# Performance work log

Measured on AMD Instinct MI355X. Metric: run time of the kernel, lower is better.

The kernel has to match this reference:

```python
import jax, jax.numpy as jnp
import numpy as np

N, D, E = 100000, 128, 1600000
BN_EPS = 1e-5

def setup_inputs() -> dict:
    key = jax.random.key(0)
    k1, k2, k3 = jax.random.split(key, 3)
    src_embeddings = jax.random.normal(k1, (N, D), dtype=jnp.float32)
    dst_embeddings = jax.random.normal(k2, (N, D), dtype=jnp.float32)
    graph = jax.random.randint(k3, (2, E), 0, N, dtype=jnp.int64)
    bn_weight = jnp.ones((1,), dtype=jnp.float32)
    bn_bias = jnp.zeros((1,), dtype=jnp.float32)
    return {
        "src_embeddings": src_embeddings,
        "dst_embeddings": dst_embeddings,
        "graph": graph,
        "bn_weight": bn_weight,
        "bn_bias": bn_bias,
    }

def reference(src_embeddings, dst_embeddings, graph, bn_weight, bn_bias):
    # gather endpoint embeddings by edge indices: [E, D]
    src = src_embeddings[graph[0]]
    dst = dst_embeddings[graph[1]]
    # squared distance per edge, clamped as in torch .clamp(min=1e-12)
    d2 = jnp.clip(jnp.sum((src - dst) ** 2, axis=-1), 1e-12, None)  # [E]
    likelihood = -jnp.log(d2)
    # BatchNorm1d(1) in training mode: batch mean, biased variance, eps=1e-5
    mu = jnp.mean(likelihood)
    var = jnp.mean((likelihood - mu) ** 2)
    edge_weights_logits = bn_weight[0] * (likelihood - mu) * jax.lax.rsqrt(var + BN_EPS) + bn_bias[0]
    # weighting_function = torch.sigmoid
    edge_weights = jax.nn.sigmoid(edge_weights_logits)
    # normalize=True: divide by mean
    edge_weights = edge_weights / jnp.mean(edge_weights)
    edge_weights = edge_weights[:, None]  # [E, 1]
    return graph, edge_weights, edge_weights_logits
```

## Files before the change

kernel.cpp:

```cpp
#include <hip/hip_runtime.h>
#include <math.h>

#define EMB_D 128
#define BN_EPS 1e-5f
#define GATHER_BLOCKS 2048
#define OVF_CAP 8192

typedef float v2f __attribute__((ext_vector_type(2)));

#if defined(__has_builtin)
#if __has_builtin(__builtin_amdgcn_cvt_pk_f32_fp8) && __has_builtin(__builtin_amdgcn_cvt_pk_fp8_f32)
#define FP8_HW 1
#endif
#endif

__device__ __forceinline__ unsigned int sw_f32_to_fp8(float x) {
    unsigned int u = __float_as_uint(x);
    unsigned int s = u >> 31;
    int e = (int)((u >> 23) & 0xff) - 127;
    unsigned int m = u & 0x7fffff;
    m += 0x7FFFF + ((m >> 20) & 1);
    if (m >> 23) { m = 0; e += 1; }
    int e8 = e + 7;
    if (e8 <= 0) return s << 7;
    if (e8 >= 15) return (s << 7) | 0x7E;
    return (s << 7) | ((unsigned)e8 << 3) | (m >> 20);
}

__device__ __forceinline__ float sw_fp8_to_f32(unsigned int v) {
    unsigned int s = (v >> 7) & 1, e = (v >> 3) & 15, m = v & 7;
    if (e == 0) return 0.0f;
    unsigned int bits = (s << 31) | ((e - 7 + 127) << 23) | (m << 20);
    return __uint_as_float(bits);
}

__device__ __forceinline__ unsigned int pack4_fp8(float4 v) {
#ifdef FP8_HW
    unsigned int o = 0;
    o = (unsigned int)__builtin_amdgcn_cvt_pk_fp8_f32(v.x, v.y, (int)o, false);
    o = (unsigned int)__builtin_amdgcn_cvt_pk_fp8_f32(v.z, v.w, (int)o, true);
    return o;
#else
    return sw_f32_to_fp8(v.x) | (sw_f32_to_fp8(v.y) << 8) |
           (sw_f32_to_fp8(v.z) << 16) | (sw_f32_to_fp8(v.w) << 24);
#endif
}

__device__ __forceinline__ float fp8x4_d2(unsigned int ua, unsigned int ub) {
#ifdef FP8_HW
    v2f a0 = __builtin_amdgcn_cvt_pk_f32_fp8((int)ua, false);
    v2f a1 = __builtin_amdgcn_cvt_pk_f32_fp8((int)ua, true);
    v2f b0 = __builtin_amdgcn_cvt_pk_f32_fp8((int)ub, false);
    v2f b1 = __builtin_amdgcn_cvt_pk_f32_fp8((int)ub, true);
    float dx = a0.x - b0.x, dy = a0.y - b0.y;
    float dz = a1.x - b1.x, dw = a1.y - b1.y;
#else
    float dx = sw_fp8_to_f32(ua & 0xff)         - sw_fp8_to_f32(ub & 0xff);
    float dy = sw_fp8_to_f32((ua >> 8) & 0xff)  - sw_fp8_to_f32((ub >> 8) & 0xff);
    float dz = sw_fp8_to_f32((ua >> 16) & 0xff) - sw_fp8_to_f32((ub >> 16) & 0xff);
    float dw = sw_fp8_to_f32(ua >> 24)          - sw_fp8_to_f32(ub >> 24);
#endif
    return fmaf(dx, dx, fmaf(dy, dy, fmaf(dz, dz, dw * dw)));
}

__device__ __forceinline__ float chunk_d2(uint4 a, uint4 b) {
    return fp8x4_d2(a.x, b.x) + fp8x4_d2(a.y, b.y)
         + fp8x4_d2(a.z, b.z) + fp8x4_d2(a.w, b.w);
}

__device__ __forceinline__ float edge_L(const unsigned char* src8,
                                        const unsigned char* dst8,
                                        int s, int d, int sub) {
    const uint4* sa = (const uint4*)(src8 + (long long)s * 128) + sub * 4;
    const uint4* sb = (const uint4*)(dst8 + (long long)d * 128) + sub * 4;
    const uint4 a0 = sa[0], a1 = sa[1], a2 = sa[2], a3 = sa[3];
    const uint4 b0 = sb[0], b1 = sb[1], b2 = sb[2], b3 = sb[3];
    float p = chunk_d2(a0, b0) + chunk_d2(a1, b1)
            + chunk_d2(a2, b2) + chunk_d2(a3, b3);
    p += __shfl_xor(p, 1, 64);
    return -logf(fmaxf(p, 1e-12f));
}

__device__ __forceinline__ unsigned int flat_to_rec(unsigned int f,
                                                    const unsigned int (&pre)[9],
                                                    unsigned int cap) {
    unsigned int j = 0, pj = 0;
    #pragma unroll
    for (int k = 1; k < 8; ++k) {
        const bool ge = (f >= pre[k]);
        j  = ge ? (unsigned int)k : j;
        pj = ge ? pre[k] : pj;
    }
    return j * cap + (f - pj);
}

__global__ void prep_bin_kernel(const float* __restrict__ src,
                                const float* __restrict__ dst,
                                unsigned int* __restrict__ src8,
                                unsigned int* __restrict__ dst8,
                                long long nElem,
                                const int* __restrict__ g,
                                long long E,
                                float* __restrict__ out_graph,
                                unsigned long long* __restrict__ rec,
                                unsigned int* __restrict__ cursors,
                                unsigned int cap,
                                float inv_slice)
{
    {
        const long long nthreads = (long long)gridDim.x * blockDim.x;
        const long long tid0 = (long long)blockIdx.x * blockDim.x + threadIdx.x;
        const long long nvec = nElem / 4;
        for (long long i = tid0; i < nvec; i += nthreads)
            src8[i] = pack4_fp8(((const float4*)src)[i]);
        for (long long i = tid0; i < nvec; i += nthreads)
            dst8[i] = pack4_fp8(((const float4*)dst)[i]);
    }

    __shared__ unsigned int hist[64];
    __shared__ unsigned int curs[64];

    const long long chunkSz = (long long)blockDim.x * 8;
    const long long nchunks = (E + chunkSz - 1) / chunkSz;

    for (long long c = blockIdx.x; c < nchunks; c += gridDim.x) {
        const long long base = c * chunkSz;
        if (threadIdx.x < 64) hist[threadIdx.x] = 0;
        __syncthreads();

        int bb[8];
        unsigned long long pk[8];
        #pragma unroll
        for (int k = 0; k < 8; ++k) {
            const long long e = base + (long long)k * blockDim.x + threadIdx.x;
            bb[k] = -1;
            if (e < E) {
                const unsigned int s = (unsigned int)g[e];
                const unsigned int d = (unsigned int)g[E + e];
                out_graph[e]     = (float)s;
                out_graph[E + e] = (float)d;
                int bs = (int)((float)s * inv_slice); bs = bs > 7 ? 7 : bs;
                int bd = (int)((float)d * inv_slice); bd = bd > 7 ? 7 : bd;
                bb[k] = bs * 8 + bd;
                pk[k] = (unsigned long long)s | ((unsigned long long)d << 20)
                      | ((unsigned long long)e << 40);
                atomicAdd(&hist[bb[k]], 1u);
            }
        }
        __syncthreads();
        if (threadIdx.x < 64 && hist[threadIdx.x] > 0)
            curs[threadIdx.x] = atomicAdd(&cursors[threadIdx.x], hist[threadIdx.x]);
        __syncthreads();

        #pragma unroll
        for (int k = 0; k < 8; ++k) {
            if (bb[k] >= 0) {
                unsigned int off = atomicAdd(&curs[bb[k]], 1u);
                if (off < cap) {
                    rec[(unsigned int)bb[k] * cap + off] = pk[k];
                } else {
                    unsigned int oo = atomicAdd(&cursors[64], 1u);
                    if (oo < OVF_CAP) rec[64u * cap + oo] = pk[k];
                }
            }
        }
        __syncthreads();
    }
}

__global__ void edge_l_binned2_kernel(const unsigned char* __restrict__ src8,
                                      const unsigned char* __restrict__ dst8,
                                      const unsigned long long* __restrict__ rec,
                                      const unsigned int* __restrict__ cursors,
                                      unsigned int cap,
                                      float* __restrict__ l_out,
                                      double* __restrict__ acc)
{
    const int tid = threadIdx.x;
    const int sub = tid & 7;
    const int grp = tid >> 3;
    const int xcd = blockIdx.x & 7;
    const unsigned int local = blockIdx.x >> 3;
    const unsigned int nloc  = gridDim.x >> 3;

    unsigned int pre[9];
    pre[0] = 0;
    #pragma unroll
    for (int j = 0; j < 8; ++j) {
        unsigned int c = cursors[xcd * 8 + j];
        if (c > cap) c = cap;
        pre[j + 1] = pre[j] + c;
    }
    const unsigned int M = pre[8];
    const unsigned long long recBase = (unsigned long long)(xcd * 8) * cap;

    double sumL = 0.0, sumL2 = 0.0;

    const unsigned int perBlock = 64;
    const unsigned int stride = nloc * perBlock;

    for (unsigned int f0 = local * perBlock; f0 < M; f0 += stride) {
        const unsigned int f1 = f0 + (unsigned int)grp;
        const unsigned int f2 = f1 + 32u;
        const bool ok1 = f1 < M;
        const bool ok2 = f2 < M;

        unsigned long long v1 = 0ull, v2 = 0ull;
        if (ok1) v1 = rec[recBase + flat_to_rec(f1, pre, cap)];
        if (ok2) v2 = rec[recBase + flat_to_rec(f2, pre, cap)];

        const int s1 = (int)(v1 & 0xFFFFFu);
        const int d1 = (int)((v1 >> 20) & 0xFFFFFu);
        const int s2 = (int)(v2 & 0xFFFFFu);
        const int d2i = (int)((v2 >> 20) & 0xFFFFFu);

        const uint4 A1 = ((const uint4*)(src8 + (long long)s1 * 128))[sub];
        const uint4 B1 = ((const uint4*)(dst8 + (long long)d1 * 128))[sub];
        const uint4 A2 = ((const uint4*)(src8 + (long long)s2 * 128))[sub];
        const uint4 B2 = ((const uint4*)(dst8 + (long long)d2i * 128))[sub];

        float p1 = chunk_d2(A1, B1);
        float p2 = chunk_d2(A2, B2);

        p1 += __shfl_xor(p1, 1, 64);
        p1 += __shfl_xor(p1, 2, 64);
        p1 += __shfl_xor(p1, 4, 64);
        p2 += __shfl_xor(p2, 1, 64);
        p2 += __shfl_xor(p2, 2, 64);
        p2 += __shfl_xor(p2, 4, 64);

        if (sub == 0) {
            if (ok1) {
                const float L = -logf(fmaxf(p1, 1e-12f));
                __builtin_nontemporal_store(L, &l_out[(long long)(v1 >> 40)]);
                sumL  += (double)L;
                sumL2 += (double)L * (double)L;
            }
            if (ok2) {
                const float L = -logf(fmaxf(p2, 1e-12f));
                __builtin_nontemporal_store(L, &l_out[(long long)(v2 >> 40)]);
                sumL  += (double)L;
                sumL2 += (double)L * (double)L;
            }
        }
    }

    {
        unsigned int ovfN = cursors[64];
        if (ovfN > OVF_CAP) ovfN = OVF_CAP;
        const unsigned long long obase = 64ull * cap;
        const unsigned int gstride = gridDim.x * 32u;
        for (unsigned int f = blockIdx.x * 32u + (unsigned int)grp;
             f < ovfN; f += gstride) {
            const unsigned long long v = rec[obase + f];
            const int s = (int)(v & 0xFFFFFu);
            const int d = (int)((v >> 20) & 0xFFFFFu);
            const uint4 A = ((const uint4*)(src8 + (long long)s * 128))[sub];
            const uint4 B = ((const uint4*)(dst8 + (long long)d * 128))[sub];
            float p = chunk_d2(A, B);
            p += __shfl_xor(p, 1, 64);
            p += __shfl_xor(p, 2, 64);
            p += __shfl_xor(p, 4, 64);
            if (sub == 0) {
                const float L = -logf(fmaxf(p, 1e-12f));
                __builtin_nontemporal_store(L, &l_out[(long long)(v >> 40)]);
                sumL  += (double)L;
                sumL2 += (double)L * (double)L;
            }
        }
    }

    __shared__ double sA[256];
    __shared__ double sB[256];
    sA[tid] = sumL;
    sB[tid] = sumL2;
    __syncthreads();
    for (int ofs = 128; ofs >= 1; ofs >>= 1) {
        if (tid < ofs) {
            sA[tid] += sA[tid + ofs];
            sB[tid] += sB[tid + ofs];
        }
        __syncthreads();
    }
    if (tid == 0) {
        atomicAdd(&acc[0], sA[0]);
        atomicAdd(&acc[1], sB[0]);
    }
}

__global__ void prep_tables_kernel(const float* __restrict__ src,
                                   const float* __restrict__ dst,
                                   unsigned int* __restrict__ src8,
                                   unsigned int* __restrict__ dst8,
                                   long long nElem)
{
    const long long nthreads = (long long)gridDim.x * blockDim.x;
    const long long tid0 = (long long)blockIdx.x * blockDim.x + threadIdx.x;
    const long long nvec = nElem / 4;
    for (long long i = tid0; i < nvec; i += nthreads)
        src8[i] = pack4_fp8(((const float4*)src)[i]);
    for (long long i = tid0; i < nvec; i += nthreads)
        dst8[i] = pack4_fp8(((const float4*)dst)[i]);
}

__global__ void edge_l_fp8_kernel(const unsigned char* __restrict__ src8,
                                  const unsigned char* __restrict__ dst8,
                                  const int* __restrict__ g,
                                  long long E,
                                  float*  __restrict__ l_out,
                                  double* __restrict__ acc)
{
    const int sub = threadIdx.x & 1;
    const int eg  = threadIdx.x >> 1;
    const long long stride = (long long)gridDim.x * 128;

    double sumL = 0.0, sumL2 = 0.0;

    long long e = (long long)blockIdx.x * 128 + eg;
    int s = 0, d = 0;
    if (e < E) { s = g[e]; d = g[E + e]; }

    while (e < E) {
        const long long en = e + stride;
        int sn = 0, dn = 0;
        if (en < E) { sn = g[en]; dn = g[E + en]; }
        const float L = edge_L(src8, dst8, s, d, sub);
        if (sub == 0) {
            l_out[e] = L;
            sumL  += (double)L;
            sumL2 += (double)L * (double)L;
        }
        e = en; s = sn; d = dn;
    }

    __shared__ double sA[256];
    __shared__ double sB[256];
    sA[threadIdx.x] = sumL;
    sB[threadIdx.x] = sumL2;
    __syncthreads();
    for (int ofs = 128; ofs >= 1; ofs >>= 1) {
        if ((int)threadIdx.x < ofs) {
            sA[threadIdx.x] += sA[threadIdx.x + ofs];
            sB[threadIdx.x] += sB[threadIdx.x + ofs];
        }
        __syncthreads();
    }
    if (threadIdx.x == 0) {
        atomicAdd(&acc[0], sA[0]);
        atomicAdd(&acc[1], sB[0]);
    }
}

__global__ void edge_l_kernel(const float* __restrict__ src,
                              const float* __restrict__ dst,
                              const int*   __restrict__ g,
                              long long E,
                              float*  __restrict__ l_out,
                              double* __restrict__ acc)
{
    const int sub  = threadIdx.x & 7;
    const int egrp = threadIdx.x >> 3;
    const long long stride = (long long)gridDim.x * 32;

    double sumL = 0.0, sumL2 = 0.0;

    long long e = (long long)blockIdx.x * 32 + egrp;
    int s = 0, d = 0;
    if (e < E) { s = g[e]; d = g[E + e]; }

    while (e < E) {
        const long long en = e + stride;
        int sn = 0, dn = 0;
        if (en < E) { sn = g[en]; dn = g[E + en]; }

        const float4* sa = (const float4*)(src + (long long)s * EMB_D);
        const float4* sb = (const float4*)(dst + (long long)d * EMB_D);
        const float4 a0 = sa[sub];      const float4 b0 = sb[sub];
        const float4 a1 = sa[sub + 8];  const float4 b1 = sb[sub + 8];
        const float4 a2 = sa[sub + 16]; const float4 b2 = sb[sub + 16];
        const float4 a3 = sa[sub + 24]; const float4 b3 = sb[sub + 24];

        float dx, dy, dz, dw, p = 0.f;
        dx = a0.x-b0.x; dy = a0.y-b0.y; dz = a0.z-b0.z; dw = a0.w-b0.w;
        p += fmaf(dx,dx,fmaf(dy,dy,fmaf(dz,dz,dw*dw)));
        dx = a1.x-b1.x; dy = a1.y-b1.y; dz = a1.z-b1.z; dw = a1.w-b1.w;
        p += fmaf(dx,dx,fmaf(dy,dy,fmaf(dz,dz,dw*dw)));
        dx = a2.x-b2.x; dy = a2.y-b2.y; dz = a2.z-b2.z; dw = a2.w-b2.w;
        p += fmaf(dx,dx,fmaf(dy,dy,fmaf(dz,dz,dw*dw)));
        dx = a3.x-b3.x; dy = a3.y-b3.y; dz = a3.z-b3.z; dw = a3.w-b3.w;
        p += fmaf(dx,dx,fmaf(dy,dy,fmaf(dz,dz,dw*dw)));

        p += __shfl_xor(p, 1, 64);
        p += __shfl_xor(p, 2, 64);
        p += __shfl_xor(p, 4, 64);

        if (sub == 0) {
            const float L = -logf(fmaxf(p, 1e-12f));
            l_out[e] = L;
            sumL  += (double)L;
            sumL2 += (double)L * (double)L;
        }
        e = en; s = sn; d = dn;
    }

    __shared__ double sA[256];
    __shared__ double sB[256];
    sA[threadIdx.x] = sumL;
    sB[threadIdx.x] = sumL2;
    __syncthreads();
    for (int ofs = 128; ofs >= 1; ofs >>= 1) {
        if ((int)threadIdx.x < ofs) {
            sA[threadIdx.x] += sA[threadIdx.x + ofs];
            sB[threadIdx.x] += sB[threadIdx.x + ofs];
        }
        __syncthreads();
    }
    if (threadIdx.x == 0) {
        atomicAdd(&acc[0], sA[0]);
        atomicAdd(&acc[1], sB[0]);
    }
}

__global__ void bn_sig_kernel(float* __restrict__ logits,
                              float* __restrict__ ew,
                              const double* __restrict__ acc,
                              double* __restrict__ sig_acc,
                              const float* __restrict__ bn_w,
                              const float* __restrict__ bn_b,
                              long long E)
{
    const long long nthreads = (long long)gridDim.x * blockDim.x;
    const long long tid0 = (long long)blockIdx.x * blockDim.x + threadIdx.x;

    __shared__ float s_mu, s_inv, s_w, s_b;
    if (threadIdx.x == 0) {
        const double mu  = acc[0] / (double)E;
        const double var = acc[1] / (double)E - mu * mu;
        s_mu  = (float)mu;
        s_inv = (float)(1.0 / sqrt(var + (double)BN_EPS));
        s_w   = bn_w[0];
        s_b   = bn_b[0];
    }
    __syncthreads();
    const float mu = s_mu, inv = s_inv, w = s_w, b = s_b;

    double sig = 0.0;
    const long long nvec = E / 4;
    for (long long i = tid0; i < nvec; i += nthreads) {
        float4 L = ((const float4*)logits)[i];
        float4 z;
        z.x = w * (L.x - mu) * inv + b;
        z.y = w * (L.y - mu) * inv + b;
        z.z = w * (L.z - mu) * inv + b;
        z.w = w * (L.w - mu) * inv + b;
        ((float4*)logits)[i] = z;
        float4 sg;
        sg.x = 1.0f / (1.0f + expf(-z.x));
        sg.y = 1.0f / (1.0f + expf(-z.y));
        sg.z = 1.0f / (1.0f + expf(-z.z));
        sg.w = 1.0f / (1.0f + expf(-z.w));
        ((float4*)ew)[i] = sg;
        sig += (double)(sg.x + sg.y) + (double)(sg.z + sg.w);
    }
    for (long long i = nvec * 4 + tid0; i < E; i += nthreads) {
        const float L = logits[i];
        const float z = w * (L - mu) * inv + b;
        logits[i] = z;
        const float sg = 1.0f / (1.0f + expf(-z));
        ew[i] = sg;
        sig += (double)sg;
    }

    __shared__ double sS[256];
    sS[threadIdx.x] = sig;
    __syncthreads();
    for (int ofs = 128; ofs >= 1; ofs >>= 1) {
        if ((int)threadIdx.x < ofs)
            sS[threadIdx.x] += sS[threadIdx.x + ofs];
        __syncthreads();
    }
    if (threadIdx.x == 0)
        atomicAdd(sig_acc, sS[0]);
}

__global__ void norm_kernel(float* __restrict__ ew,
                            const double* __restrict__ sig_acc,
                            const int* __restrict__ g,
                            float* __restrict__ out_graph,
                            int do_graph,
                            long long E)
{
    const long long nthreads = (long long)gridDim.x * blockDim.x;
    const long long tid0 = (long long)blockIdx.x * blockDim.x + threadIdx.x;
    const float scale = (float)((double)E / sig_acc[0]);

    const long long nvec = E / 4;
    for (long long i = tid0; i < nvec; i += nthreads) {
        float4 v = ((const float4*)ew)[i];
        v.x *= scale; v.y *= scale; v.z *= scale; v.w *= scale;
        ((float4*)ew)[i] = v;
    }
    for (long long i = nvec * 4 + tid0; i < E; i += nthreads)
        ew[i] *= scale;

    if (do_graph) {
        const long long gvec = (2 * E) / 4;
        for (long long i = tid0; i < gvec; i += nthreads) {
            const int4 v = ((const int4*)g)[i];
            float4 f;
            f.x = (float)v.x; f.y = (float)v.y; f.z = (float)v.z; f.w = (float)v.w;
            ((float4*)out_graph)[i] = f;
        }
        for (long long i = gvec * 4 + tid0; i < 2 * E; i += nthreads)
            out_graph[i] = (float)g[i];
    }
}

extern "C" void kernel_launch(void* const* d_in, const int* in_sizes, int n_in,
                              void* d_out, int out_size, void* d_ws, size_t ws_size,
                              hipStream_t stream) {
    const float* src  = (const float*)d_in[0];
    const float* dst  = (const float*)d_in[1];
    const int*   g    = (const int*)d_in[2];
    const float* bn_w = (const float*)d_in[3];
    const float* bn_b = (const float*)d_in[4];

    const long long N = (long long)in_sizes[0] / EMB_D;
    const long long E = (long long)in_sizes[2] / 2;

    float* out        = (float*)d_out;
    float* out_graph  = out;
    float* out_ew     = out + 2 * E;
    float* out_logits = out + 3 * E;

    double*       acc     = (double*)d_ws;
    unsigned int* cursors = (unsigned int*)((char*)d_ws + 64);
    unsigned char* src8   = (unsigned char*)d_ws + 512;
    unsigned char* dst8   = src8 + (size_t)N * EMB_D;
    unsigned long long* rec = (unsigned long long*)(dst8 + (size_t)N * EMB_D);

    const unsigned int cap = (unsigned int)(E / 64 + 2048);
    const size_t need_full = 512 + (size_t)N * EMB_D * 2
                           + ((size_t)64 * cap + OVF_CAP) * 8;
    const size_t need_fp8  = 512 + (size_t)N * EMB_D * 2;

    const int slice_sz = (int)((N + 7) / 8);
    const float inv_slice = 1.0f / (float)slice_sz;

    hipMemsetAsync(d_ws, 0, 512, stream);

    if (ws_size >= need_full && N < (1 << 20) && E < (1LL << 24)) {
        prep_bin_kernel<<<4096, 256, 0, stream>>>(src, dst,
                                                  (unsigned int*)src8,
                                                  (unsigned int*)dst8,
                                                  N * EMB_D, g, E, out_graph,
                                                  rec, cursors, cap, inv_slice);
        edge_l_binned2_kernel<<<GATHER_BLOCKS, 256, 0, stream>>>(
            src8, dst8, rec, cursors, cap, out_logits, acc);
        bn_sig_kernel<<<1024, 256, 0, stream>>>(out_logits, out_ew, acc, &acc[2],
                                                bn_w, bn_b, E);
        norm_kernel<<<1024, 256, 0, stream>>>(out_ew, &acc[2], g, out_graph, 0, E);
    } else if (ws_size >= need_fp8) {
        prep_tables_kernel<<<4096, 256, 0, stream>>>(src, dst,
                                                     (unsigned int*)src8,
                                                     (unsigned int*)dst8,
                                                     N * EMB_D);
        edge_l_fp8_kernel<<<4096, 256, 0, stream>>>(src8, dst8, g, E,
                                                    out_logits, acc);
        bn_sig_kernel<<<1024, 256, 0, stream>>>(out_logits, out_ew, acc, &acc[2],
                                                bn_w, bn_b, E);
        norm_kernel<<<1024, 256, 0, stream>>>(out_ew, &acc[2], g, out_graph, 1, E);
    } else {
        edge_l_kernel<<<4096, 256, 0, stream>>>(src, dst, g, E, out_logits, acc);
        bn_sig_kernel<<<1024, 256, 0, stream>>>(out_logits, out_ew, acc, &acc[2],
                                                bn_w, bn_b, E);
        norm_kernel<<<1024, 256, 0, stream>>>(out_ew, &acc[2], g, out_graph, 1, E);
    }
}
```

Baseline: 262.6 us.

## Unroll binned gather to four edges, recompute sigmoid in normalize pass

The binned gather kernel now processes four edges per 8-lane group per iteration instead of two, with twice the grid size, so more independent gathers are in flight. The BN/sigmoid kernel no longer writes sigmoid values and only accumulates their sum. The normalize kernel then recomputes the sigmoid from the logits and writes scaled weights with nontemporal stores. Graph output writes in the binning kernel also become nontemporal. This trades one extra exp per element for one fewer E-sized write and read pass, at the cost of more register pressure in the gather kernel.

```diff
diff --git a/kernel.cpp b/kernel.cpp
--- a/kernel.cpp
+++ b/kernel.cpp
@@ -3,10 +3,11 @@
 
 #define EMB_D 128
 #define BN_EPS 1e-5f
-#define GATHER_BLOCKS 2048
+#define GATHER_BLOCKS 4096
 #define OVF_CAP 8192
 
 typedef float v2f __attribute__((ext_vector_type(2)));
+typedef float v4f __attribute__((ext_vector_type(4)));
 
 #if defined(__has_builtin)
 #if __has_builtin(__builtin_amdgcn_cvt_pk_f32_fp8) && __has_builtin(__builtin_amdgcn_cvt_pk_fp8_f32)
@@ -137,8 +138,8 @@
             if (e < E) {
                 const unsigned int s = (unsigned int)g[e];
                 const unsigned int d = (unsigned int)g[E + e];
-                out_graph[e]     = (float)s;
-                out_graph[E + e] = (float)d;
+                __builtin_nontemporal_store((float)s, &out_graph[e]);
+                __builtin_nontemporal_store((float)d, &out_graph[E + e]);
                 int bs = (int)((float)s * inv_slice); bs = bs > 7 ? 7 : bs;
                 int bd = (int)((float)d * inv_slice); bd = bd > 7 ? 7 : bd;
                 bb[k] = bs * 8 + bd;
@@ -168,7 +169,7 @@
     }
 }
 
-__global__ void edge_l_binned2_kernel(const unsigned char* __restrict__ src8,
+__global__ void edge_l_binned3_kernel(const unsigned char* __restrict__ src8,
                                       const unsigned char* __restrict__ dst8,
                                       const unsigned long long* __restrict__ rec,
                                       const unsigned int* __restrict__ cursors,
@@ -196,51 +197,51 @@
 
     double sumL = 0.0, sumL2 = 0.0;
 
-    const unsigned int perBlock = 64;
+    const unsigned int perBlock = 128;
     const unsigned int stride = nloc * perBlock;
 
     for (unsigned int f0 = local * perBlock; f0 < M; f0 += stride) {
-        const unsigned int f1 = f0 + (unsigned int)grp;
-        const unsigned int f2 = f1 + 32u;
-        const bool ok1 = f1 < M;
-        const bool ok2 = f2 < M;
-
-        unsigned long long v1 = 0ull, v2 = 0ull;
-        if (ok1) v1 = rec[recBase + flat_to_rec(f1, pre, cap)];
-        if (ok2) v2 = rec[recBase + flat_to_rec(f2, pre, cap)];
-
-        const int s1 = (int)(v1 & 0xFFFFFu);
-        const int d1 = (int)((v1 >> 20) & 0xFFFFFu);
-        const int s2 = (int)(v2 & 0xFFFFFu);
-        const int d2i = (int)((v2 >> 20) & 0xFFFFFu);
-
-        const uint4 A1 = ((const uint4*)(src8 + (long long)s1 * 128))[sub];
-        const uint4 B1 = ((const uint4*)(dst8 + (long long)d1 * 128))[sub];
-        const uint4 A2 = ((const uint4*)(src8 + (long long)s2 * 128))[sub];
-        const uint4 B2 = ((const uint4*)(dst8 + (long long)d2i * 128))[sub];
-
-        float p1 = chunk_d2(A1, B1);
-        float p2 = chunk_d2(A2, B2);
-
-        p1 += __shfl_xor(p1, 1, 64);
-        p1 += __shfl_xor(p1, 2, 64);
-        p1 += __shfl_xor(p1, 4, 64);
-        p2 += __shfl_xor(p2, 1, 64);
-        p2 += __shfl_xor(p2, 2, 64);
-        p2 += __shfl_xor(p2, 4, 64);
+        unsigned int ff[4];
+        bool ok[4];
+        unsigned long long v[4];
+        #pragma unroll
+        for (int k = 0; k < 4; ++k) {
+            ff[k] = f0 + (unsigned int)grp + 32u * (unsigned int)k;
+            ok[k] = ff[k] < M;
+            v[k] = 0ull;
+            if (ok[k]) v[k] = rec[recBase + flat_to_rec(ff[k], pre, cap)];
+        }
+
+        uint4 A[4], B[4];
+        #pragma unroll
+        for (int k = 0; k < 4; ++k) {
+            const int s = (int)(v[k] & 0xFFFFFu);
+            const int d = (int)((v[k] >> 20) & 0xFFFFFu);
+            A[k] = ((const uint4*)(src8 + (long long)s * 128))[sub];
+            B[k] = ((const uint4*)(dst8 + (long long)d * 128))[sub];
+        }
+
+        float p[4];
+        #pragma unroll
+        for (int k = 0; k < 4; ++k)
+            p[k] = chunk_d2(A[k], B[k]);
+
+        #pragma unroll
+        for (int k = 0; k < 4; ++k) {
+            p[k] += __shfl_xor(p[k], 1, 64);
+            p[k] += __shfl_xor(p[k], 2, 64);
+            p[k] += __shfl_xor(p[k], 4, 64);
+        }
 
         if (sub == 0) {
-            if (ok1) {
-                const float L = -logf(fmaxf(p1, 1e-12f));
-                __builtin_nontemporal_store(L, &l_out[(long long)(v1 >> 40)]);
-                sumL  += (double)L;
-                sumL2 += (double)L * (double)L;
-            }
-            if (ok2) {
-                const float L = -logf(fmaxf(p2, 1e-12f));
-                __builtin_nontemporal_store(L, &l_out[(long long)(v2 >> 40)]);
-                sumL  += (double)L;
-                sumL2 += (double)L * (double)L;
+            #pragma unroll
+            for (int k = 0; k < 4; ++k) {
+                if (ok[k]) {
+                    const float L = -logf(fmaxf(p[k], 1e-12f));
+                    __builtin_nontemporal_store(L, &l_out[(long long)(v[k] >> 40)]);
+                    sumL  += (double)L;
+                    sumL2 += (double)L * (double)L;
+                }
             }
         }
     }
@@ -255,9 +256,9 @@
             const unsigned long long v = rec[obase + f];
             const int s = (int)(v & 0xFFFFFu);
             const int d = (int)((v >> 20) & 0xFFFFFu);
-            const uint4 A = ((const uint4*)(src8 + (long long)s * 128))[sub];
-            const uint4 B = ((const uint4*)(dst8 + (long long)d * 128))[sub];
-            float p = chunk_d2(A, B);
+            const uint4 Av = ((const uint4*)(src8 + (long long)s * 128))[sub];
+            const uint4 Bv = ((const uint4*)(dst8 + (long long)d * 128))[sub];
+            float p = chunk_d2(Av, Bv);
             p += __shfl_xor(p, 1, 64);
             p += __shfl_xor(p, 2, 64);
             p += __shfl_xor(p, 4, 64);
@@ -422,7 +423,6 @@
 }
 
 __global__ void bn_sig_kernel(float* __restrict__ logits,
-                              float* __restrict__ ew,
                               const double* __restrict__ acc,
                               double* __restrict__ sig_acc,
                               const float* __restrict__ bn_w,
@@ -454,21 +454,17 @@
         z.z = w * (L.z - mu) * inv + b;
         z.w = w * (L.w - mu) * inv + b;
         ((float4*)logits)[i] = z;
-        float4 sg;
-        sg.x = 1.0f / (1.0f + expf(-z.x));
-        sg.y = 1.0f / (1.0f + expf(-z.y));
-        sg.z = 1.0f / (1.0f + expf(-z.z));
-        sg.w = 1.0f / (1.0f + expf(-z.w));
-        ((float4*)ew)[i] = sg;
-        sig += (double)(sg.x + sg.y) + (double)(sg.z + sg.w);
+        const float sx = 1.0f / (1.0f + expf(-z.x));
+        const float sy = 1.0f / (1.0f + expf(-z.y));
+        const float sz = 1.0f / (1.0f + expf(-z.z));
+        const float sw2 = 1.0f / (1.0f + expf(-z.w));
+        sig += (double)(sx + sy) + (double)(sz + sw2);
     }
     for (long long i = nvec * 4 + tid0; i < E; i += nthreads) {
         const float L = logits[i];
         const float z = w * (L - mu) * inv + b;
         logits[i] = z;
-        const float sg = 1.0f / (1.0f + expf(-z));
-        ew[i] = sg;
-        sig += (double)sg;
+        sig += (double)(1.0f / (1.0f + expf(-z)));
     }
 
     __shared__ double sS[256];
@@ -483,7 +479,8 @@
         atomicAdd(sig_acc, sS[0]);
 }
 
-__global__ void norm_kernel(float* __restrict__ ew,
+__global__ void norm_kernel(const float* __restrict__ logits,
+                            float* __restrict__ ew,
                             const double* __restrict__ sig_acc,
                             const int* __restrict__ g,
                             float* __restrict__ out_graph,
@@ -496,12 +493,16 @@
 
     const long long nvec = E / 4;
     for (long long i = tid0; i < nvec; i += nthreads) {
-        float4 v = ((const float4*)ew)[i];
-        v.x *= scale; v.y *= scale; v.z *= scale; v.w *= scale;
-        ((float4*)ew)[i] = v;
+        const float4 z = ((const float4*)logits)[i];
+        v4f v;
+        v.x = scale / (1.0f + expf(-z.x));
+        v.y = scale / (1.0f + expf(-z.y));
+        v.z = scale / (1.0f + expf(-z.z));
+        v.w = scale / (1.0f + expf(-z.w));
+        __builtin_nontemporal_store(v, (v4f*)ew + i);
     }
     for (long long i = nvec * 4 + tid0; i < E; i += nthreads)
-        ew[i] *= scale;
+        ew[i] = scale / (1.0f + expf(-logits[i]));
 
     if (do_graph) {
         const long long gvec = (2 * E) / 4;
@@ -547,7 +548,7 @@
     const int slice_sz = (int)((N + 7) / 8);
     const float inv_slice = 1.0f / (float)slice_sz;
 
-    hipMemsetAsync(d_ws, 0, 512, stream);
+    (void)hipMemsetAsync(d_ws, 0, 512, stream);
 
     if (ws_size >= need_full && N < (1 << 20) && E < (1LL << 24)) {
         prep_bin_kernel<<<4096, 256, 0, stream>>>(src, dst,
@@ -555,11 +556,12 @@
                                                   (unsigned int*)dst8,
                                                   N * EMB_D, g, E, out_graph,
                                                   rec, cursors, cap, inv_slice);
-        edge_l_binned2_kernel<<<GATHER_BLOCKS, 256, 0, stream>>>(
+        edge_l_binned3_kernel<<<GATHER_BLOCKS, 256, 0, stream>>>(
             src8, dst8, rec, cursors, cap, out_logits, acc);
-        bn_sig_kernel<<<1024, 256, 0, stream>>>(out_logits, out_ew, acc, &acc[2],
+        bn_sig_kernel<<<1024, 256, 0, stream>>>(out_logits, acc, &acc[2],
                                                 bn_w, bn_b, E);
-        norm_kernel<<<1024, 256, 0, stream>>>(out_ew, &acc[2], g, out_graph, 0, E);
+        norm_kernel<<<1024, 256, 0, stream>>>(out_logits, out_ew, &acc[2],
+                                              g, out_graph, 0, E);
     } else if (ws_size >= need_fp8) {
         prep_tables_kernel<<<4096, 256, 0, stream>>>(src, dst,
                                                      (unsigned int*)src8,
@@ -567,13 +569,15 @@
                                                      N * EMB_D);
         edge_l_fp8_kernel<<<4096, 256, 0, stream>>>(src8, dst8, g, E,
                                                     out_logits, acc);
-        bn_sig_kernel<<<1024, 256, 0, stream>>>(out_logits, out_ew, acc, &acc[2],
+        bn_sig_kernel<<<1024, 256, 0, stream>>>(out_logits, acc, &acc[2],
                                                 bn_w, bn_b, E);
-        norm_kernel<<<1024, 256, 0, stream>>>(out_ew, &acc[2], g, out_graph, 1, E);
+        norm_kernel<<<1024, 256, 0, stream>>>(out_logits, out_ew, &acc[2],
+                                              g, out_graph, 1, E);
     } else {
         edge_l_kernel<<<4096, 256, 0, stream>>>(src, dst, g, E, out_logits, acc);
-        bn_sig_kernel<<<1024, 256, 0, stream>>>(out_logits, out_ew, acc, &acc[2],
+        bn_sig_kernel<<<1024, 256, 0, stream>>>(out_logits, acc, &acc[2],
                                                 bn_w, bn_b, E);
-        norm_kernel<<<1024, 256, 0, stream>>>(out_ew, &acc[2], g, out_graph, 1, E);
-    }
-}
+        norm_kernel<<<1024, 256, 0, stream>>>(out_logits, out_ew, &acc[2],
+                                              g, out_graph, 1, E);
+    }
+}
```

After: 291.3 us. +10.9%, slower.
